# Optimization experiments

Hardware: AMD Instinct MI355X
Metric: run time of the kernel (lower is better)

The kernel has to match this reference:

```python
import jax, jax.numpy as jnp
import numpy as np

NUM_ANCHORS = 2
NUM_CLASSES = 20
H = 7
W = 7
IMG_H = 448
IMG_W = 448
NMS_THRESH = 0.7
SCORE_THRESH = 0.05
NBOX = H * W * NUM_ANCHORS  # 98 candidate boxes per image


def _format_outputs(x):
    # x: [b, H*W*(num_anchors*5 + num_classes)] -> decoded boxes/objectness/scores
    b = x.shape[0]
    x = x.reshape(b, H, W, NUM_ANCHORS * 5 + NUM_CLASSES)
    # class scores shared across anchors of a cell (repeat_interleave in torch)
    b_scores = jnp.broadcast_to(
        x[..., -NUM_CLASSES:].reshape(b, H * W, 1, NUM_CLASSES),
        (b, H * W, NUM_ANCHORS, NUM_CLASSES),
    )
    xa = x[..., : NUM_ANCHORS * 5].reshape(b, H, W, NUM_ANCHORS, 5)
    c_x = jnp.arange(W, dtype=x.dtype) * (IMG_W / W)
    c_y = jnp.arange(H, dtype=x.dtype) * (IMG_H / H)
    b_x = jax.nn.sigmoid(xa[..., 0]) + c_x[None, None, :, None]
    b_y = jax.nn.sigmoid(xa[..., 1]) + c_y[None, :, None, None]
    b_w = jax.nn.sigmoid(xa[..., 2])
    b_h = jax.nn.sigmoid(xa[..., 3])
    b_coords = jnp.stack((b_x, b_y, b_w, b_h), axis=-1).reshape(b, H * W, NUM_ANCHORS, 4)
    b_o = jax.nn.sigmoid(xa[..., 4]).reshape(b, H * W, NUM_ANCHORS)
    return b_coords, b_o, b_scores


def _pairwise_iou(boxes):
    # boxes: [n, 4] xyxy -> [n, n] IoU (torchvision box_iou semantics, 0 where union==0)
    area = (boxes[:, 2] - boxes[:, 0]) * (boxes[:, 3] - boxes[:, 1])
    lt = jnp.maximum(boxes[:, None, :2], boxes[None, :, :2])
    rb = jnp.minimum(boxes[:, None, 2:], boxes[None, :, 2:])
    wh = jnp.clip(rb - lt, 0.0)
    inter = wh[..., 0] * wh[..., 1]
    union = area[:, None] + area[None, :] - inter
    return jnp.where(union > 0, inter / union, 0.0)


def _per_image(coords, o, sc):
    # coords: [NBOX,4] (x,y,w,h), o: [NBOX], sc: [NBOX,NUM_CLASSES]
    valid = o >= 0.5  # objectness gate (b_o >= 0.5 selection in torch)
    labels = jnp.argmax(sc, axis=-1)
    scores = jnp.max(sc, axis=-1)
    # xywh -> xyxy, clamp to [0,1] (as in post_process)
    boxes = jnp.clip(
        jnp.concatenate([coords[:, :2], coords[:, :2] + coords[:, 2:]], axis=-1), 0.0, 1.0
    )
    # sort by score descending, invalid boxes pushed to the end
    s = jnp.where(valid, scores, -jnp.inf)
    order = jnp.argsort(-s)
    boxes_s = boxes[order]
    scores_s = scores[order]
    labels_s = labels[order]
    valid_s = valid[order]
    iou = _pairwise_iou(boxes_s)
    idxs = jnp.arange(NBOX)

    def body(i, alive):
        # if box i is still alive, suppress later boxes with IoU > thresh
        suppress = (iou[i] > NMS_THRESH) & (idxs > i) & alive[i]
        return alive & ~suppress

    alive = jax.lax.fori_loop(0, NBOX, body, valid_s)
    keep = alive & (scores_s >= SCORE_THRESH)
    boxes_out = jnp.where(keep[:, None], boxes_s, 0.0)
    scores_out = jnp.where(keep, scores_s, 0.0)
    labels_out = jnp.where(keep, labels_s, 0)
    return boxes_out, scores_out, labels_out, keep


def setup_inputs() -> dict:
    key = jax.random.key(0)
    x = jax.random.normal(key, (8192, H * W * (NUM_ANCHORS * 5 + NUM_CLASSES)), dtype=jnp.float32)
    return {"x": x}


def reference(x):
    b_coords, b_o, b_scores = _format_outputs(x)
    b = x.shape[0]
    coords = b_coords.reshape(b, -1, 4)
    o = b_o.reshape(b, -1)
    sc = b_scores.reshape(b, -1, NUM_CLASSES)
    boxes, scores, labels, keep = jax.vmap(_per_image)(coords, o, sc)
    # padded detections: [b, NBOX, 4], [b, NBOX], [b, NBOX], keep mask [b, NBOX]
    return boxes, scores, labels, keep
```

## Files before the change

### kernel.cpp

```cpp
#include <hip/hip_runtime.h>
#include <math.h>

#define NBOX 98
#define ROWLEN 1470
#define NMS_T 0.7f
#define SCORE_T 0.05f

__device__ __forceinline__ float psigm(float v) {
    return 1.0f / (1.0f + expf(-v));
}
__device__ __forceinline__ float fsigm(float v) {
    return __builtin_amdgcn_rcpf(1.0f + __expf(-v));
}

__device__ __forceinline__ void gl_lds16(const float4* g, float4* l) {
    __builtin_amdgcn_global_load_lds((const __attribute__((address_space(1))) void*)g,
                                     (__attribute__((address_space(3))) void*)l,
                                     16, 0, 0);
}

__global__ __launch_bounds__(128) void yolo_post(const float* __restrict__ x,
                                                 float* __restrict__ out,
                                                 int batch) {
    const int wid  = threadIdx.x >> 6;
    const int lane = threadIdx.x & 63;
    const int b    = blockIdx.x * 2 + wid;

    __shared__ __align__(16) float srow[2 * ROWLEN + 4];

    {
        const float4* gsrc = reinterpret_cast<const float4*>(
            x + (size_t)blockIdx.x * (2 * ROWLEN));
        float4* lrow = reinterpret_cast<float4*>(srow);
        const size_t maxq = ((size_t)batch * ROWLEN) >> 2;
        const size_t qbase = (size_t)blockIdx.x * ((2 * ROWLEN) / 4);
        #pragma unroll
        for (int r = 0; r < 6; ++r) {
            const int idx = r * 128 + threadIdx.x;
            if (idx < 735 && qbase + (size_t)idx < maxq) {
                gl_lds16(gsrc + idx, lrow + (r * 128 + wid * 64));
            }
        }
    }
    __syncthreads();
    if (b >= batch) return;

    const float* row = srow + wid * ROWLEN;

    const int  cell   = lane;
    const bool active = (cell < 49);

    float  s = 0.0f, lab = 0.0f;
    int    vbits = 0;
    float4 B0 = make_float4(1.f, 1.f, 1.f, 1.f);
    float4 B1 = make_float4(1.f, 1.f, 1.f, 1.f);

    if (active) {
        const float* c = row + cell * 30;
        float mx = c[10]; int ml = 0;
        #pragma unroll
        for (int t = 1; t < 20; ++t) {
            const float v = c[10 + t];
            if (v > mx) { mx = v; ml = t; }
        }
        s = mx; lab = (float)ml;

        const int ci = cell / 7;
        const int cj = cell - ci * 7;

        if (c[4] >= 0.0f) vbits |= 1;
        if (c[9] >= 0.0f) vbits |= 2;

        const float sx0 = fsigm(c[0]), sy0 = fsigm(c[1]);
        const float sw0 = fsigm(c[2]), sh0 = fsigm(c[3]);
        const float sx1 = fsigm(c[5]), sy1 = fsigm(c[6]);
        const float sw1 = fsigm(c[7]), sh1 = fsigm(c[8]);

        if (cj == 0) {
            B0.x = fminf(fmaxf(sx0, 0.f), 1.f);
            B0.z = fminf(fmaxf(sx0 + sw0, 0.f), 1.f);
            B1.x = fminf(fmaxf(sx1, 0.f), 1.f);
            B1.z = fminf(fmaxf(sx1 + sw1, 0.f), 1.f);
        }
        if (ci == 0) {
            B0.y = fminf(fmaxf(sy0, 0.f), 1.f);
            B0.w = fminf(fmaxf(sy0 + sh0, 0.f), 1.f);
            B1.y = fminf(fmaxf(sy1, 0.f), 1.f);
            B1.w = fminf(fmaxf(sy1 + sh1, 0.f), 1.f);
        }
    }

    const bool v0 = (vbits & 1) != 0;
    const bool v1 = (vbits & 2) != 0;
    const int  cnt = (vbits & 1) + (vbits >> 1);

    const unsigned long long V0m = __ballot(v0);
    const unsigned long long V1m = __ballot(v1);
    const int V = (int)__popcll(V0m) + (int)__popcll(V1m);

    bool kill_local = false;
    if (cell == 0 && (vbits & 3) == 3) {
        const float a0 = (B0.z - B0.x) * (B0.w - B0.y);
        const float a1 = (B1.z - B1.x) * (B1.w - B1.y);
        const float w  = fmaxf(fminf(B0.z, B1.z) - fmaxf(B0.x, B1.x), 0.f);
        const float h  = fmaxf(fminf(B0.w, B1.w) - fmaxf(B0.y, B1.y), 0.f);
        const float inter = w * h;
        const float uni   = a0 + a1 - inter;
        const float delta = inter - NMS_T * uni;
        if (fabsf(delta) < 1e-4f * uni) {
            const float px0 = psigm(row[0]), py0 = psigm(row[1]);
            const float pw0 = psigm(row[2]), ph0 = psigm(row[3]);
            const float px1 = psigm(row[5]), py1 = psigm(row[6]);
            const float pw1 = psigm(row[7]), ph1 = psigm(row[8]);
            const float X0 = fminf(fmaxf(px0, 0.f), 1.f), Y0 = fminf(fmaxf(py0, 0.f), 1.f);
            const float Z0 = fminf(fmaxf(px0 + pw0, 0.f), 1.f), W0 = fminf(fmaxf(py0 + ph0, 0.f), 1.f);
            const float X1 = fminf(fmaxf(px1, 0.f), 1.f), Y1 = fminf(fmaxf(py1, 0.f), 1.f);
            const float Z1 = fminf(fmaxf(px1 + pw1, 0.f), 1.f), W1 = fminf(fmaxf(py1 + ph1, 0.f), 1.f);
            const float pa0 = (Z0 - X0) * (W0 - Y0);
            const float pa1 = (Z1 - X1) * (W1 - Y1);
            const float pw  = fmaxf(fminf(Z0, Z1) - fmaxf(X0, X1), 0.f);
            const float ph  = fmaxf(fminf(W0, W1) - fmaxf(Y0, Y1), 0.f);
            const float pint = pw * ph;
            const float puni = pa0 + pa1 - pint;
            const float iou  = (puni > 0.f) ? (pint / puni) : 0.f;
            kill_local = (iou > NMS_T);
        } else {
            kill_local = (delta > 0.f);
        }
    }
    const bool kill1 = (__ballot(kill_local) != 0ull);

    const int ib = __float_as_int(s);
    const unsigned uo = (unsigned)ib ^ (unsigned)((ib >> 31) | 0x80000000);
    const unsigned long long key =
        ((unsigned long long)uo << 8) | ((unsigned)(63 - cell) << 2) | (unsigned)cnt;
    const unsigned klo = (unsigned)key;
    const unsigned khi = (unsigned)(key >> 32);

    int acc0 = 0, acc1 = 0, acc2 = 0, acc3 = 0;
    #pragma unroll
    for (int j = 0; j < 49; ++j) {
        const unsigned jlo = (unsigned)__builtin_amdgcn_readlane((int)klo, j);
        const unsigned jhi = (unsigned)__builtin_amdgcn_readlane((int)khi, j);
        const unsigned long long kj = ((unsigned long long)jhi << 32) | jlo;
        const int cj_ = (int)(jlo & 3u);
        const int add = (kj > key) ? cj_ : 0;
        if ((j & 3) == 0) acc0 += add;
        else if ((j & 3) == 1) acc1 += add;
        else if ((j & 3) == 2) acc2 += add;
        else acc3 += add;
    }
    const int rcom = (acc0 + acc1) + (acc2 + acc3);

    const unsigned long long below = (1ull << cell) - 1ull;
    const int prefv = (int)__popcll(V0m & below) + (int)__popcll(V1m & below);

    const int r0 = v0 ? rcom
                      : (V + 2 * cell - prefv);
    const int r1 = v1 ? (rcom + (v0 ? 1 : 0))
                      : (V + 2 * cell + 1 - prefv - (v0 ? 1 : 0));

    const bool k0 = v0 && (s >= SCORE_T);
    const bool k1 = v1 && (s >= SCORE_T) && !(kill1 && cell == 0);

    if (active) {
        float4* boxes = reinterpret_cast<float4*>(out + (size_t)b * (NBOX * 4));
        const size_t base1 = (size_t)batch * (NBOX * 4);
        const size_t bn    = (size_t)batch * NBOX;
        float* scores = out + base1 +          (size_t)b * NBOX;
        float* labels = out + base1 + bn +     (size_t)b * NBOX;
        float* keepm  = out + base1 + 2 * bn + (size_t)b * NBOX;

        const float4 z = make_float4(0.f, 0.f, 0.f, 0.f);
        boxes[r0]  = k0 ? B0 : z;
        boxes[r1]  = k1 ? B1 : z;
        scores[r0] = k0 ? s : 0.f;
        scores[r1] = k1 ? s : 0.f;
        labels[r0] = k0 ? lab : 0.f;
        labels[r1] = k1 ? lab : 0.f;
        keepm[r0]  = k0 ? 1.f : 0.f;
        keepm[r1]  = k1 ? 1.f : 0.f;
    }
}

extern "C" void kernel_launch(void* const* d_in, const int* in_sizes, int n_in,
                              void* d_out, int out_size, void* d_ws, size_t ws_size,
                              hipStream_t stream) {
    const float* x = (const float*)d_in[0];
    float* out = (float*)d_out;
    const int batch = in_sizes[0] / ROWLEN;
    const int grid  = (batch + 1) / 2;
    yolo_post<<<grid, 128, 0, stream>>>(x, out, batch);
}
```

Before: 98.75 us.

## Process two images per wave with register prefetch overlapping LDS load

Each wave now handles two images: one row is loaded straight into LDS asynchronously, while the second is prefetched into registers and computed after the first. The block-wide barrier is replaced by per-wave waitcnt and wave barriers, and each wave's LDS slot is padded so misaligned rows can be read with an offset. The grid is halved. The aim is to hide global-load latency behind computation and cut block and barrier overhead, at the cost of more registers and fewer waves for the scheduler to interleave.

```diff
diff --git a/kernel.cpp b/kernel.cpp
--- a/kernel.cpp
+++ b/kernel.cpp
@@ -3,6 +3,7 @@
 
 #define NBOX 98
 #define ROWLEN 1470
+#define WLDSF 1472
 #define NMS_T 0.7f
 #define SCORE_T 0.05f
 
@@ -19,34 +20,8 @@
                                      16, 0, 0);
 }
 
-__global__ __launch_bounds__(128) void yolo_post(const float* __restrict__ x,
-                                                 float* __restrict__ out,
-                                                 int batch) {
-    const int wid  = threadIdx.x >> 6;
-    const int lane = threadIdx.x & 63;
-    const int b    = blockIdx.x * 2 + wid;
-
-    __shared__ __align__(16) float srow[2 * ROWLEN + 4];
-
-    {
-        const float4* gsrc = reinterpret_cast<const float4*>(
-            x + (size_t)blockIdx.x * (2 * ROWLEN));
-        float4* lrow = reinterpret_cast<float4*>(srow);
-        const size_t maxq = ((size_t)batch * ROWLEN) >> 2;
-        const size_t qbase = (size_t)blockIdx.x * ((2 * ROWLEN) / 4);
-        #pragma unroll
-        for (int r = 0; r < 6; ++r) {
-            const int idx = r * 128 + threadIdx.x;
-            if (idx < 735 && qbase + (size_t)idx < maxq) {
-                gl_lds16(gsrc + idx, lrow + (r * 128 + wid * 64));
-            }
-        }
-    }
-    __syncthreads();
-    if (b >= batch) return;
-
-    const float* row = srow + wid * ROWLEN;
-
+__device__ __forceinline__ void process(const float* __restrict__ row, int b, int lane,
+                                        float* __restrict__ out, int batch) {
     const int  cell   = lane;
     const bool active = (cell < 49);
 
@@ -155,8 +130,7 @@
     const unsigned long long below = (1ull << cell) - 1ull;
     const int prefv = (int)__popcll(V0m & below) + (int)__popcll(V1m & below);
 
-    const int r0 = v0 ? rcom
-                      : (V + 2 * cell - prefv);
+    const int r0 = v0 ? rcom : (V + 2 * cell - prefv);
     const int r1 = v1 ? (rcom + (v0 ? 1 : 0))
                       : (V + 2 * cell + 1 - prefv - (v0 ? 1 : 0));
 
@@ -183,12 +157,76 @@
     }
 }
 
+__global__ __launch_bounds__(128) void yolo_post(const float* __restrict__ x,
+                                                 float* __restrict__ out,
+                                                 int batch) {
+    const int wid  = threadIdx.x >> 6;
+    const int lane = threadIdx.x & 63;
+    const int W    = (batch + 1) >> 1;
+    const int gw   = blockIdx.x * 2 + wid;
+
+    __shared__ __align__(16) float srow[2 * WLDSF];
+    float* wbase = srow + wid * WLDSF;
+    float4* ldst = reinterpret_cast<float4*>(wbase);
+    const float4* gq = reinterpret_cast<const float4*>(x);
+    const size_t totalQ = ((size_t)batch * ROWLEN) >> 2;
+
+    const int imgA = gw;
+    const int imgB = gw + W;
+
+    const size_t eoffA = (size_t)imgA * ROWLEN;
+    const size_t eoffB = (size_t)imgB * ROWLEN;
+    const int  remA = (int)(eoffA & 3);
+    const int  remB = (int)(eoffB & 3);
+    const size_t qA = eoffA >> 2;
+    const size_t qB = eoffB >> 2;
+
+    if (imgA < batch) {
+        #pragma unroll
+        for (int r = 0; r < 6; ++r) {
+            const int slot = r * 64 + lane;
+            if (slot < 368 && qA + (size_t)slot < totalQ)
+                gl_lds16(gq + qA + slot, ldst + slot);
+        }
+    }
+    float4 pf[6];
+    if (imgB < batch) {
+        #pragma unroll
+        for (int r = 0; r < 6; ++r) {
+            const int slot = r * 64 + lane;
+            if (slot < 368 && qB + (size_t)slot < totalQ)
+                pf[r] = gq[qB + slot];
+        }
+    }
+
+    __builtin_amdgcn_s_waitcnt(0x0F70);
+    __builtin_amdgcn_wave_barrier();
+
+    if (imgA < batch) process(wbase + remA, imgA, lane, out, batch);
+
+    __builtin_amdgcn_s_waitcnt(0xC07F);
+    __builtin_amdgcn_wave_barrier();
+
+    if (imgB < batch) {
+        #pragma unroll
+        for (int r = 0; r < 6; ++r) {
+            const int slot = r * 64 + lane;
+            if (slot < 368 && qB + (size_t)slot < totalQ)
+                ldst[slot] = pf[r];
+        }
+        __builtin_amdgcn_s_waitcnt(0xC07F);
+        __builtin_amdgcn_wave_barrier();
+        process(wbase + remB, imgB, lane, out, batch);
+    }
+}
+
 extern "C" void kernel_launch(void* const* d_in, const int* in_sizes, int n_in,
                               void* d_out, int out_size, void* d_ws, size_t ws_size,
                               hipStream_t stream) {
     const float* x = (const float*)d_in[0];
     float* out = (float*)d_out;
     const int batch = in_sizes[0] / ROWLEN;
-    const int grid  = (batch + 1) / 2;
+    const int W     = (batch + 1) / 2;
+    const int grid  = (W + 1) / 2;
     yolo_post<<<grid, 128, 0, stream>>>(x, out, batch);
 }
```

New measurement: 108.3 us. 9.7% more time.

## Replace LDS staging with direct per-lane vector global loads, four images per block

Applied to the files above, without the earlier changes.

Drops the global_load_lds staging of two image rows into shared memory and the block barrier that followed it. Each lane now reads its own cell's 30 floats straight from global memory with float2/float4 loads. Blocks grow to 256 threads and process four images each. This removes the LDS round trip and the synchronisation. In exchange, the per-lane loads use a 120-byte stride and many are not 16-byte aligned, so coalescing may suffer.

```diff
diff --git a/kernel.cpp b/kernel.cpp
--- a/kernel.cpp
+++ b/kernel.cpp
@@ -13,68 +13,52 @@
     return __builtin_amdgcn_rcpf(1.0f + __expf(-v));
 }
 
-__device__ __forceinline__ void gl_lds16(const float4* g, float4* l) {
-    __builtin_amdgcn_global_load_lds((const __attribute__((address_space(1))) void*)g,
-                                     (__attribute__((address_space(3))) void*)l,
-                                     16, 0, 0);
-}
-
-__global__ __launch_bounds__(128) void yolo_post(const float* __restrict__ x,
+__global__ __launch_bounds__(256) void yolo_post(const float* __restrict__ x,
                                                  float* __restrict__ out,
                                                  int batch) {
     const int wid  = threadIdx.x >> 6;
     const int lane = threadIdx.x & 63;
-    const int b    = blockIdx.x * 2 + wid;
-
-    __shared__ __align__(16) float srow[2 * ROWLEN + 4];
-
-    {
-        const float4* gsrc = reinterpret_cast<const float4*>(
-            x + (size_t)blockIdx.x * (2 * ROWLEN));
-        float4* lrow = reinterpret_cast<float4*>(srow);
-        const size_t maxq = ((size_t)batch * ROWLEN) >> 2;
-        const size_t qbase = (size_t)blockIdx.x * ((2 * ROWLEN) / 4);
-        #pragma unroll
-        for (int r = 0; r < 6; ++r) {
-            const int idx = r * 128 + threadIdx.x;
-            if (idx < 735 && qbase + (size_t)idx < maxq) {
-                gl_lds16(gsrc + idx, lrow + (r * 128 + wid * 64));
-            }
-        }
-    }
-    __syncthreads();
-    if (b >= batch) return;
-
-    const float* row = srow + wid * ROWLEN;
+    const int img  = blockIdx.x * 4 + wid;
+    if (img >= batch) return;
 
     const int  cell   = lane;
     const bool active = (cell < 49);
 
-    float  s = 0.0f, lab = 0.0f;
-    int    vbits = 0;
+    const float* c = x + (size_t)img * ROWLEN + (active ? cell : 0) * 30;
+
+    const float2 d0  = *reinterpret_cast<const float2*>(c);
+    const float4 d1  = *reinterpret_cast<const float4*>(c + 2);
+    const float4 d2  = *reinterpret_cast<const float4*>(c + 6);
+    const float4 q0  = *reinterpret_cast<const float4*>(c + 10);
+    const float4 q1  = *reinterpret_cast<const float4*>(c + 14);
+    const float4 q2  = *reinterpret_cast<const float4*>(c + 18);
+    const float4 q3  = *reinterpret_cast<const float4*>(c + 22);
+    const float4 q4  = *reinterpret_cast<const float4*>(c + 26);
+
+    float cls[20] = {q0.x,q0.y,q0.z,q0.w, q1.x,q1.y,q1.z,q1.w,
+                     q2.x,q2.y,q2.z,q2.w, q3.x,q3.y,q3.z,q3.w,
+                     q4.x,q4.y,q4.z,q4.w};
+    float mx = cls[0]; int ml = 0;
+    #pragma unroll
+    for (int t = 1; t < 20; ++t) {
+        if (cls[t] > mx) { mx = cls[t]; ml = t; }
+    }
+    const float s   = active ? mx : 0.0f;
+    const float lab = (float)ml;
+
+    int vbits = 0;
     float4 B0 = make_float4(1.f, 1.f, 1.f, 1.f);
     float4 B1 = make_float4(1.f, 1.f, 1.f, 1.f);
-
     if (active) {
-        const float* c = row + cell * 30;
-        float mx = c[10]; int ml = 0;
-        #pragma unroll
-        for (int t = 1; t < 20; ++t) {
-            const float v = c[10 + t];
-            if (v > mx) { mx = v; ml = t; }
-        }
-        s = mx; lab = (float)ml;
-
         const int ci = cell / 7;
         const int cj = cell - ci * 7;
+        if (d1.z >= 0.0f) vbits |= 1;
+        if (d2.w >= 0.0f) vbits |= 2;
 
-        if (c[4] >= 0.0f) vbits |= 1;
-        if (c[9] >= 0.0f) vbits |= 2;
-
-        const float sx0 = fsigm(c[0]), sy0 = fsigm(c[1]);
-        const float sw0 = fsigm(c[2]), sh0 = fsigm(c[3]);
-        const float sx1 = fsigm(c[5]), sy1 = fsigm(c[6]);
-        const float sw1 = fsigm(c[7]), sh1 = fsigm(c[8]);
+        const float sx0 = fsigm(d0.x), sy0 = fsigm(d0.y);
+        const float sw0 = fsigm(d1.x), sh0 = fsigm(d1.y);
+        const float sx1 = fsigm(d1.w), sy1 = fsigm(d2.x);
+        const float sw1 = fsigm(d2.y), sh1 = fsigm(d2.z);
 
         if (cj == 0) {
             B0.x = fminf(fmaxf(sx0, 0.f), 1.f);
@@ -108,10 +92,10 @@
         const float uni   = a0 + a1 - inter;
         const float delta = inter - NMS_T * uni;
         if (fabsf(delta) < 1e-4f * uni) {
-            const float px0 = psigm(row[0]), py0 = psigm(row[1]);
-            const float pw0 = psigm(row[2]), ph0 = psigm(row[3]);
-            const float px1 = psigm(row[5]), py1 = psigm(row[6]);
-            const float pw1 = psigm(row[7]), ph1 = psigm(row[8]);
+            const float px0 = psigm(d0.x), py0 = psigm(d0.y);
+            const float pw0 = psigm(d1.x), ph0 = psigm(d1.y);
+            const float px1 = psigm(d1.w), py1 = psigm(d2.x);
+            const float pw1 = psigm(d2.y), ph1 = psigm(d2.z);
             const float X0 = fminf(fmaxf(px0, 0.f), 1.f), Y0 = fminf(fmaxf(py0, 0.f), 1.f);
             const float Z0 = fminf(fmaxf(px0 + pw0, 0.f), 1.f), W0 = fminf(fmaxf(py0 + ph0, 0.f), 1.f);
             const float X1 = fminf(fmaxf(px1, 0.f), 1.f), Y1 = fminf(fmaxf(py1, 0.f), 1.f);
@@ -155,8 +139,7 @@
     const unsigned long long below = (1ull << cell) - 1ull;
     const int prefv = (int)__popcll(V0m & below) + (int)__popcll(V1m & below);
 
-    const int r0 = v0 ? rcom
-                      : (V + 2 * cell - prefv);
+    const int r0 = v0 ? rcom : (V + 2 * cell - prefv);
     const int r1 = v1 ? (rcom + (v0 ? 1 : 0))
                       : (V + 2 * cell + 1 - prefv - (v0 ? 1 : 0));
 
@@ -164,12 +147,12 @@
     const bool k1 = v1 && (s >= SCORE_T) && !(kill1 && cell == 0);
 
     if (active) {
-        float4* boxes = reinterpret_cast<float4*>(out + (size_t)b * (NBOX * 4));
+        float4* boxes = reinterpret_cast<float4*>(out + (size_t)img * (NBOX * 4));
         const size_t base1 = (size_t)batch * (NBOX * 4);
         const size_t bn    = (size_t)batch * NBOX;
-        float* scores = out + base1 +          (size_t)b * NBOX;
-        float* labels = out + base1 + bn +     (size_t)b * NBOX;
-        float* keepm  = out + base1 + 2 * bn + (size_t)b * NBOX;
+        float* scores = out + base1 +          (size_t)img * NBOX;
+        float* labels = out + base1 + bn +     (size_t)img * NBOX;
+        float* keepm  = out + base1 + 2 * bn + (size_t)img * NBOX;
 
         const float4 z = make_float4(0.f, 0.f, 0.f, 0.f);
         boxes[r0]  = k0 ? B0 : z;
@@ -189,6 +172,6 @@
     const float* x = (const float*)d_in[0];
     float* out = (float*)d_out;
     const int batch = in_sizes[0] / ROWLEN;
-    const int grid  = (batch + 1) / 2;
-    yolo_post<<<grid, 128, 0, stream>>>(x, out, batch);
+    const int grid  = (batch + 3) / 4;
+    yolo_post<<<grid, 256, 0, stream>>>(x, out, batch);
 }
```

Measured after the change: 100.4 us. No clear change (+1.6%).
